# Performance work log

Measured on AMD Instinct MI355X. Metric: run time of the kernel, lower is better.

The kernel has to match this reference:

```python
import jax, jax.numpy as jnp
import numpy as np

NUM_EXPERTS = 16
IN_FEATURES = 512
OUT_FEATURES = 512
N_TOKENS = 2048


def setup_inputs() -> dict:
    key = jax.random.key(0)
    k_x, k_idx, k_w, k_b = jax.random.split(key, 4)
    x = jax.random.normal(k_x, (N_TOKENS, IN_FEATURES), dtype=jnp.float32)
    indices = jax.random.randint(k_idx, (N_TOKENS,), 0, NUM_EXPERTS, dtype=jnp.int64)
    # nn.Linear default init: U(-1/sqrt(in), 1/sqrt(in)) for weight [out,in] and bias [out]
    bound = 1.0 / np.sqrt(IN_FEATURES)
    W = jax.random.uniform(k_w, (NUM_EXPERTS, OUT_FEATURES, IN_FEATURES),
                           minval=-bound, maxval=bound, dtype=jnp.float32)
    b = jax.random.uniform(k_b, (NUM_EXPERTS, OUT_FEATURES),
                           minval=-bound, maxval=bound, dtype=jnp.float32)
    return {"x": x, "indices": indices, "W": W, "b": b}


def reference(x, indices, W, b):
    # Faithful to SwitchLinear.forward: gather per-token expert weight/bias,
    # then per-token GEMV (batched matmul with a length-1 row dim).
    w_tok = W[indices]            # [N, out, in]  (naive per-token weight gather)
    b_tok = b[indices]            # [N, out]
    out = jnp.einsum('ni,noi->no', x, w_tok) + b_tok  # [N, out]
    return out
```

## Files before the change

### kernel.cpp

```cpp
#include <hip/hip_runtime.h>
#include <hip/hip_bf16.h>

#define NE    16
#define INF   512
#define OUTF  512
#define NT    2048
#define OTILE 32
#define TCH   32
#define NZ    2
#define LSTRIDE 520

#define SZ_W   (OTILE * LSTRIDE * 2)
#define SZ_X   (TCH * LSTRIDE * 2)
#define SZ_LST ((NT + TCH) * 4)
#define SMEM_BYTES (SZ_W + SZ_X + SZ_LST + 64)

typedef __attribute__((ext_vector_type(4))) float f32x4;
typedef __attribute__((ext_vector_type(8))) short bf16x8;
typedef __attribute__((ext_vector_type(4))) short bf16x4;

__device__ inline unsigned short f2bf(float f) {
    union { __hip_bfloat16 h; unsigned short s; } u;
    u.h = __float2bfloat16(f);
    return u.s;
}

__device__ inline bf16x4 cvt4(f32x4 v) {
    bf16x4 r;
    r[0] = (short)f2bf(v[0]); r[1] = (short)f2bf(v[1]);
    r[2] = (short)f2bf(v[2]); r[3] = (short)f2bf(v[3]);
    return r;
}

__global__ __launch_bounds__(256, 2)
void switch_linear_kernel(const float* __restrict__ x,
                          const int* __restrict__ idx,
                          const float* __restrict__ W,
                          const float* __restrict__ bias,
                          float* __restrict__ out)
{
    extern __shared__ char smem[];
    short* s_W    = (short*)smem;
    short* s_X    = (short*)(smem + SZ_W);
    int*   s_list = (int*)(smem + SZ_W + SZ_X);
    int*   s_wcnt = (int*)(smem + SZ_W + SZ_X + SZ_LST);

    const int b   = blockIdx.x;
    const int e   = b & 15;
    const int oj  = (b >> 4) & 15;
    const int o0  = oj * OTILE;
    const int z   = b >> 8;
    const int tid = threadIdx.x;
    const int lane = tid & 63;
    const int wv   = tid >> 6;

    int iv[8];
#pragma unroll
    for (int it = 0; it < 8; ++it)
        iv[it] = idx[wv * 512 + it * 64 + lane];

    const float* wbase = W + ((size_t)e * OUTF + o0) * INF;
#pragma unroll
    for (int i = 0; i < 16; ++i) {
        const int li = tid + i * 256;
        f32x4 v = ((const f32x4*)wbase)[li];
        const int row = li >> 7;
        const int col = (li * 4) & 511;
        *(bf16x4*)(&s_W[row * LSTRIDE + col]) = cvt4(v);
    }

    unsigned long long masks[8];
    int wtot = 0;
#pragma unroll
    for (int it = 0; it < 8; ++it) {
        const unsigned long long mk = __ballot(iv[it] == e);
        masks[it] = mk;
        wtot += __popcll(mk);
    }
    if (lane == 0) s_wcnt[wv] = wtot;
    __syncthreads();
    int base = 0;
#pragma unroll
    for (int w = 0; w < 4; ++w) { int c = s_wcnt[w]; if (w < wv) base += c; }
    const int cnt = s_wcnt[0] + s_wcnt[1] + s_wcnt[2] + s_wcnt[3];
    const unsigned long long below = (1ull << lane) - 1ull;
    int run = base;
#pragma unroll
    for (int it = 0; it < 8; ++it) {
        const unsigned long long mk = masks[it];
        if (mk & (1ull << lane))
            s_list[run + __popcll(mk & below)] = wv * 512 + it * 64 + lane;
        run += __popcll(mk);
    }
    const int cnt_pad = (cnt + TCH - 1) & ~(TCH - 1);
    for (int i = cnt + tid; i < cnt_pad; i += 256) s_list[i] = -1;
    __syncthreads();
    if (cnt == 0) return;

    const int wt = wv >> 1;
    const int wo = wv & 1;
    const int lr = lane & 15;
    const int q  = lane >> 4;
    const int orow = o0 + wo * 16 + lr;

    bf16x8 bfr[16];
#pragma unroll
    for (int kk = 0; kk < 16; ++kk)
        bfr[kk] = *(const bf16x8*)(&s_W[(wo * 16 + lr) * LSTRIDE + kk * 32 + q * 8]);
    const float bv = bias[e * OUTF + orow];

    const int slot = tid >> 3;
    const int sub  = tid & 7;

    const int nch = cnt_pad / TCH;
    const int M = (nch - z + NZ - 1) / NZ;
    if (M <= 0) return;
    const int m0 = oj % M;

    for (int k = 0; k < M; ++k) {
        int m = m0 + k; if (m >= M) m -= M;
        const int cb = (z + m * NZ) * TCH;

        int tok_s = s_list[cb + slot];
        if (tok_s < 0) tok_s = 0;
        const f32x4* xr = (const f32x4*)(x + (size_t)tok_s * INF);
        f32x4 xreg[16];
#pragma unroll
        for (int i = 0; i < 16; ++i) xreg[i] = xr[sub + i * 8];
#pragma unroll
        for (int i = 0; i < 16; ++i)
            *(bf16x4*)(&s_X[slot * LSTRIDE + (sub + i * 8) * 4]) = cvt4(xreg[i]);
        __syncthreads();

        f32x4 acc = {0.f, 0.f, 0.f, 0.f};
#pragma unroll
        for (int kk = 0; kk < 16; ++kk) {
            bf16x8 afr = *(const bf16x8*)(&s_X[(wt * 16 + lr) * LSTRIDE + kk * 32 + q * 8]);
            acc = __builtin_amdgcn_mfma_f32_16x16x32_bf16(afr, bfr[kk], acc, 0, 0, 0);
        }
#pragma unroll
        for (int j = 0; j < 4; ++j) {
            const int tok = s_list[cb + wt * 16 + q * 4 + j];
            if (tok >= 0) out[(size_t)tok * OUTF + orow] = acc[j] + bv;
        }
        if (k != M - 1) __syncthreads();
    }
}

extern "C" void kernel_launch(void* const* d_in, const int* in_sizes, int n_in,
                              void* d_out, int out_size, void* d_ws, size_t ws_size,
                              hipStream_t stream) {
    const float* x    = (const float*)d_in[0];
    const int*   idx  = (const int*)d_in[1];
    const float* W    = (const float*)d_in[2];
    const float* bias = (const float*)d_in[3];
    float* out = (float*)d_out;

    dim3 grid(NE * 16 * NZ);
    dim3 block(256);
    switch_linear_kernel<<<grid, block, SMEM_BYTES, stream>>>(x, idx, W, bias, out);
}
```

Measured before the change: 12.97 us.

## Prefetch next token chunk into registers during MFMA and warm x into cache

Restructures the token-chunk loop so the next chunk's x rows are loaded into registers while the current chunk's MFMAs and output stores run, then converted to bf16 and written to LDS between two barriers. Also staggers the order of the weight-tile load for the second z-half and adds a dummy x prefetch per block to warm L2. The aim is to hide global load latency behind compute. It adds an extra barrier per iteration and more register pressure under a two-blocks-per-CU launch bound.

```diff
diff --git a/kernel.cpp b/kernel.cpp
--- a/kernel.cpp
+++ b/kernel.cpp
@@ -62,11 +62,20 @@
     const float* wbase = W + ((size_t)e * OUTF + o0) * INF;
 #pragma unroll
     for (int i = 0; i < 16; ++i) {
-        const int li = tid + i * 256;
+        const int ii = z ? ((i + 8) & 15) : i;
+        const int li = tid + ii * 256;
         f32x4 v = ((const f32x4*)wbase)[li];
         const int row = li >> 7;
         const int col = (li * 4) & 511;
         *(bf16x4*)(&s_W[row * LSTRIDE + col]) = cvt4(v);
+    }
+
+    {
+        const f32x4* xpf = (const f32x4*)x + (size_t)b * 512 + tid;
+        f32x4 p0 = xpf[0];
+        f32x4 p1 = xpf[256];
+        float s = p0[0] + p1[3];
+        asm volatile("" :: "v"(s));
     }
 
     unsigned long long masks[8];
@@ -117,20 +126,34 @@
     if (M <= 0) return;
     const int m0 = oj % M;
 
-    for (int k = 0; k < M; ++k) {
-        int m = m0 + k; if (m >= M) m -= M;
-        const int cb = (z + m * NZ) * TCH;
-
+    f32x4 xreg[16];
+    {
+        const int cb = (z + m0 * NZ) * TCH;
         int tok_s = s_list[cb + slot];
         if (tok_s < 0) tok_s = 0;
         const f32x4* xr = (const f32x4*)(x + (size_t)tok_s * INF);
-        f32x4 xreg[16];
 #pragma unroll
         for (int i = 0; i < 16; ++i) xreg[i] = xr[sub + i * 8];
 #pragma unroll
         for (int i = 0; i < 16; ++i)
             *(bf16x4*)(&s_X[slot * LSTRIDE + (sub + i * 8) * 4]) = cvt4(xreg[i]);
-        __syncthreads();
+    }
+    __syncthreads();
+
+    for (int k = 0; k < M; ++k) {
+        int m = m0 + k; if (m >= M) m -= M;
+        const int cb = (z + m * NZ) * TCH;
+        const bool more = (k + 1) < M;
+
+        if (more) {
+            int mn = m0 + k + 1; if (mn >= M) mn -= M;
+            const int cbn = (z + mn * NZ) * TCH;
+            int tok_s = s_list[cbn + slot];
+            if (tok_s < 0) tok_s = 0;
+            const f32x4* xr = (const f32x4*)(x + (size_t)tok_s * INF);
+#pragma unroll
+            for (int i = 0; i < 16; ++i) xreg[i] = xr[sub + i * 8];
+        }
 
         f32x4 acc = {0.f, 0.f, 0.f, 0.f};
 #pragma unroll
@@ -143,7 +166,14 @@
             const int tok = s_list[cb + wt * 16 + q * 4 + j];
             if (tok >= 0) out[(size_t)tok * OUTF + orow] = acc[j] + bv;
         }
-        if (k != M - 1) __syncthreads();
+
+        if (more) {
+            __syncthreads();
+#pragma unroll
+            for (int i = 0; i < 16; ++i)
+                *(bf16x4*)(&s_X[slot * LSTRIDE + (sub + i * 8) * 4]) = cvt4(xreg[i]);
+            __syncthreads();
+        }
     }
 }
 
```

Measured after the change: 13.40 us. 3.3% more time.
